# Kernel optimization log

Measured on AMD Instinct MI355X. Metric: run time of the kernel, lower is better.

## Reference

```python
import jax, jax.numpy as jnp
import numpy as np

N, D, H, E = 50000, 128, 128, 800000

def _layernorm(h, g, b, eps=1e-5):
    m = jnp.mean(h, axis=-1, keepdims=True)
    v = jnp.mean((h - m) ** 2, axis=-1, keepdims=True)
    return (h - m) * jax.lax.rsqrt(v + eps) * g + b

def setup_inputs() -> dict:
    key = jax.random.key(0)
    ks = jax.random.split(key, 24)
    s = 0.02
    inp = {
        "x": jax.random.normal(ks[0], (N, D), dtype=jnp.float32),
        "edge_index": jax.random.randint(ks[1], (2, E), 0, N, dtype=jnp.int64),
        "degree": jax.random.uniform(ks[2], (N, 1), dtype=jnp.float32) * 32.0,
        "W_lin": jax.random.normal(ks[3], (D, H), jnp.float32) * s,
        "b_lin": jnp.zeros((H,), jnp.float32),
        "Wa1": jax.random.normal(ks[4], (H, H), jnp.float32) * s,
        "ba1": jnp.zeros((H,), jnp.float32),
        "Wa2": jax.random.normal(ks[5], (H, H), jnp.float32) * s,
        "ba2": jnp.zeros((H,), jnp.float32),
        "Wb1": jax.random.normal(ks[6], (H, H), jnp.float32) * s,
        "bb1": jnp.zeros((H,), jnp.float32),
        "Wb2": jax.random.normal(ks[7], (H, H), jnp.float32) * s,
        "bb2": jnp.zeros((H,), jnp.float32),
        "Wg1": jax.random.normal(ks[8], (H, H), jnp.float32) * s,
        "bg1": jnp.zeros((H,), jnp.float32),
        "Wg2": jax.random.normal(ks[9], (H, H), jnp.float32) * s,
        "bg2": jnp.zeros((H,), jnp.float32),
        "Wf1": jax.random.normal(ks[10], (H, H), jnp.float32) * s,
        "bf1": jnp.zeros((H,), jnp.float32),
        "Wf2": jax.random.normal(ks[11], (H, H), jnp.float32) * s,
        "bf2": jnp.zeros((H,), jnp.float32),
        "ln_g": jnp.ones((H,), jnp.float32),
        "ln_b": jnp.zeros((H,), jnp.float32),
    }
    return inp

def reference(x, edge_index, degree, W_lin, b_lin, Wa1, ba1, Wa2, ba2,
              Wb1, bb1, Wb2, bb2, Wg1, bg1, Wg2, bg2, Wf1, bf1, Wf2, bf2,
              ln_g, ln_b):
    # Dropout layers are identity (eval mode)
    h = x @ W_lin + b_lin                                  # [N,H]
    x_res = _layernorm(h, ln_g, ln_b)
    alpha = jax.nn.softplus(jax.nn.relu(h @ Wa1 + ba1) @ Wa2 + ba2)
    beta = jax.nn.softplus(jax.nn.relu(h @ Wb1 + bb1) @ Wb2 + bb2)
    gamma = jax.nn.gelu(h @ Wg1 + bg1, approximate=False) @ Wg2 + bg2
    src, dst = edge_index[0], edge_index[1]
    agg = jax.ops.segment_sum(h[src], dst, num_segments=h.shape[0])  # [N,H]
    y = (beta * agg + gamma) / (alpha + beta * degree)
    z = jax.nn.gelu(y @ Wf1 + bf1, approximate=False) @ Wf2 + bf2
    return z + x_res
```

## Files before the change

kernel.cpp:

```cpp
#include <hip/hip_runtime.h>
#include <hip/hip_bf16.h>
#include <math.h>

#define NODES 50000
#define NEDGE 800000
#define NT_TILES 782
#define NBUCK 98
#define BSHIFT 9
#define BCAP 10240
#define NP1 195
#define EPB1 4104

typedef __bf16 bf16_t;
typedef __bf16 bf16x8 __attribute__((ext_vector_type(8)));
typedef float floatx4 __attribute__((ext_vector_type(4)));

__device__ __forceinline__ float bfbits2f(unsigned int hi16) {
    union { unsigned int u; float f; } c; c.u = hi16; return c.f;
}
__device__ __forceinline__ unsigned short f2bfbits(float f) {
    bf16_t b = (bf16_t)f; unsigned short u;
    __builtin_memcpy(&u, &b, 2); return u;
}

__device__ __forceinline__ float act_rt(float v, int act) {
    if (act == 1) return fmaxf(v, 0.f);
    if (act == 2) {
        float w = 0.79788456f * (v + 0.044715f * v * v * v);
        float e = __expf(2.f * w);
        float th = 1.f - 2.f / (e + 1.f);
        return 0.5f * v * (1.f + th);
    }
    if (act == 3) return fmaxf(v, 0.f) + __logf(1.f + __expf(-fabsf(v)));
    return v;
}

__global__ __launch_bounds__(256) void prep_w_zero(
    const float* __restrict__ w0, const float* __restrict__ w1,
    const float* __restrict__ w2, const float* __restrict__ w3,
    const float* __restrict__ w4, const float* __restrict__ w5,
    const float* __restrict__ w6, const float* __restrict__ w7,
    const float* __restrict__ w8, bf16_t* __restrict__ wt,
    int* __restrict__ gcur)
{
    if (blockIdx.x >= 9) {
        if (threadIdx.x < NBUCK) gcur[threadIdx.x] = 0;
        return;
    }
    const float* Ws[9] = {w0, w1, w2, w3, w4, w5, w6, w7, w8};
    const float* W = Ws[blockIdx.x];
    bf16_t* o = wt + blockIdx.x * 16384;
    for (int idx = threadIdx.x; idx < 16384; idx += 256) {
        int k = idx >> 7, n = idx & 127;
        o[n * 128 + k] = (bf16_t)W[idx];
    }
}

__device__ __forceinline__ void load_w_regs(const bf16_t* __restrict__ W,
                                            uint4 (&wr)[8], int t)
{
    for (int i = 0; i < 8; ++i) {
        int c = t + i * 256;
        int row = c >> 4, g = c & 15;
        wr[i] = *(const uint4*)(W + row * 128 + g * 8);
    }
}
__device__ __forceinline__ void store_w_regs(const uint4 (&wr)[8],
                                             bf16_t* Bs, int t)
{
    for (int i = 0; i < 8; ++i) {
        int c = t + i * 256;
        int row = c >> 4, g = c & 15;
        *(uint4*)&Bs[row * 128 + ((g ^ (row & 15)) * 8)] = wr[i];
    }
}
__device__ __forceinline__ void afrag_gbf16(const bf16_t* __restrict__ A,
        bf16x8 (&af)[4], int r0, int lane, int wave, int M)
{
    int gr = r0 + wave * 16 + (lane & 15);
    gr = min(gr, M - 1);
    const bf16_t* p = A + (size_t)gr * 128 + (lane >> 4) * 8;
    for (int kc = 0; kc < 4; ++kc)
        af[kc] = *(const bf16x8*)(p + kc * 32);
}
__device__ __forceinline__ void kloop64(const bf16x8 (&af)[4], const bf16_t* Bs,
                                        floatx4 (&acc)[8], int l15, int quad)
{
    for (int ni = 0; ni < 8; ++ni)
        for (int r = 0; r < 4; ++r) acc[ni][r] = 0.f;
    for (int kc = 0; kc < 4; ++kc) {
        int kg = kc * 4 + quad;
        bf16x8 b[8];
        for (int ni = 0; ni < 8; ++ni) {
            int row = ni * 16 + l15;
            b[ni] = *(const bf16x8*)&Bs[row * 128 + ((kg ^ l15) * 8)];
        }
        for (int ni = 0; ni < 8; ++ni)
            acc[ni] = __builtin_amdgcn_mfma_f32_16x16x32_bf16(
                af[kc], b[ni], acc[ni], 0, 0, 0);
    }
}
__device__ __forceinline__ void write_Csw(bf16_t* Csw, floatx4 (&acc)[8],
        const float (&bias_r)[8], int lane, int wave, int act)
{
    const int l15 = lane & 15, quad = lane >> 4;
    for (int ni = 0; ni < 8; ++ni) {
        int col = ni * 16 + l15;
        for (int r = 0; r < 4; ++r) {
            int row = wave * 16 + quad * 4 + r;
            float v = act_rt(acc[ni][r] + bias_r[ni], act);
            Csw[row * 128 + (((col >> 3) ^ (row & 15)) << 3) + (col & 7)] = (bf16_t)v;
        }
    }
}
__device__ __forceinline__ void afrag_Csw(const bf16_t* Csw, bf16x8 (&af)[4],
                                          int lane, int wave)
{
    int l15 = lane & 15, quad = lane >> 4;
    int row = wave * 16 + l15;
    for (int kc = 0; kc < 4; ++kc) {
        int kg = kc * 4 + quad;
        af[kc] = *(const bf16x8*)&Csw[row * 128 + ((kg ^ l15) * 8)];
    }
}
__device__ __forceinline__ void copy_Csw_out(const bf16_t* Csw,
        bf16_t* __restrict__ out, int t, int r0, int M)
{
    for (int i = 0; i < 4; ++i) {
        int c = t + i * 256;
        int row = c >> 4, g = c & 15;
        int gr = r0 + row;
        if (gr < M)
            *(uint4*)(out + (size_t)gr * 128 + g * 8) =
                *(const uint4*)&Csw[row * 128 + ((g ^ (row & 15)) * 8)];
    }
}

__global__ __launch_bounds__(256, 3) void hln_p1(
    const float* __restrict__ x, const bf16_t* __restrict__ wt,
    const float* __restrict__ b_lin,
    const float* __restrict__ ln_g, const float* __restrict__ ln_b,
    bf16_t* __restrict__ h, bf16_t* __restrict__ xres,
    const int* __restrict__ ei, int* __restrict__ gcur,
    unsigned* __restrict__ ebuf, int M)
{
    __shared__ __align__(16) char smem[49152];
    const int t = threadIdx.x;
    const int bid = blockIdx.x;

    if (bid % 5 == 4) {
        int* lcnt  = (int*)smem;
        int* lbase = lcnt + NBUCK;
        if (t < NBUCK) lcnt[t] = 0;
        __syncthreads();
        int p1id = bid / 5;
        int base = p1id * EPB1;
        int e_end = min(base + EPB1, NEDGE);
        for (int e = base + t; e < e_end; e += 256)
            atomicAdd(&lcnt[ei[NEDGE + e] >> BSHIFT], 1);
        __syncthreads();
        if (t < NBUCK) {
            lbase[t] = atomicAdd(&gcur[t], lcnt[t]);
            lcnt[t] = 0;
        }
        __syncthreads();
        for (int e = base + t; e < e_end; e += 256) {
            int d = ei[NEDGE + e];
            int s = ei[e];
            int b = d >> BSHIFT;
            int off = atomicAdd(&lcnt[b], 1);
            int pos = lbase[b] + off;
            if (pos < BCAP)
                ebuf[(size_t)b * BCAP + pos] =
                    (unsigned)s | ((unsigned)(d & 511) << 16);
        }
        return;
    }

    bf16_t* Bs  = (bf16_t*)smem;
    bf16_t* Csw = (bf16_t*)(smem + 32768);
    const int tile = bid - bid / 5;
    const int r0 = tile * 64;
    const int lane = t & 63, wave = t >> 6, l15 = lane & 15, quad = lane >> 4;
    uint4 wr[8];
    bf16x8 af[4];
    floatx4 acc[8];
    float bias_r[8];
    for (int ni = 0; ni < 8; ++ni) bias_r[ni] = b_lin[ni * 16 + l15];

    {
        int gr = min(r0 + wave * 16 + l15, M - 1);
        const float* p = x + (size_t)gr * 128 + quad * 8;
        for (int kc = 0; kc < 4; ++kc) {
            float4 u0 = *(const float4*)(p + kc * 32);
            float4 u1 = *(const float4*)(p + kc * 32 + 4);
            bf16x8 f;
            f[0] = (bf16_t)u0.x; f[1] = (bf16_t)u0.y;
            f[2] = (bf16_t)u0.z; f[3] = (bf16_t)u0.w;
            f[4] = (bf16_t)u1.x; f[5] = (bf16_t)u1.y;
            f[6] = (bf16_t)u1.z; f[7] = (bf16_t)u1.w;
            af[kc] = f;
        }
    }
    load_w_regs(wt, wr, t);
    store_w_regs(wr, Bs, t);
    __syncthreads();
    kloop64(af, Bs, acc, l15, quad);
    write_Csw(Csw, acc, bias_r, lane, wave, 0);
    __syncthreads();

    int row = t >> 2, p4 = t & 3;
    int gr = r0 + row;
    uint4 raw[4];
    float vals[32];
    float s = 0.f, sq = 0.f;
    for (int i = 0; i < 4; ++i) {
        int lg = p4 * 4 + i;
        raw[i] = *(const uint4*)&Csw[row * 128 + ((lg ^ (row & 15)) * 8)];
        const unsigned* u = (const unsigned*)&raw[i];
        for (int k = 0; k < 4; ++k) {
            float f0 = bfbits2f(u[k] << 16);
            float f1 = bfbits2f(u[k] & 0xffff0000u);
            vals[i * 8 + k * 2] = f0; vals[i * 8 + k * 2 + 1] = f1;
            s += f0 + f1; sq += f0 * f0 + f1 * f1;
        }
    }
    s += __shfl_xor(s, 1, 64);  sq += __shfl_xor(sq, 1, 64);
    s += __shfl_xor(s, 2, 64);  sq += __shfl_xor(sq, 2, 64);
    float m   = s * (1.f / 128.f);
    float var = fmaxf(sq * (1.f / 128.f) - m * m, 0.f);
    float rs  = rsqrtf(var + 1e-5f);
    if (gr < M) {
        for (int i = 0; i < 4; ++i) {
            int lg = p4 * 4 + i;
            *(uint4*)(h + (size_t)gr * 128 + lg * 8) = raw[i];
            unsigned short ob[8];
            for (int k = 0; k < 8; ++k) {
                int col = lg * 8 + k;
                ob[k] = f2bfbits((vals[i * 8 + k] - m) * rs * ln_g[col] + ln_b[col]);
            }
            uint4 o;
            o.x = ob[0] | ((unsigned)ob[1] << 16);
            o.y = ob[2] | ((unsigned)ob[3] << 16);
            o.z = ob[4] | ((unsigned)ob[5] << 16);
            o.w = ob[6] | ((unsigned)ob[7] << 16);
            *(uint4*)(xres + (size_t)gr * 128 + lg * 8) = o;
        }
    }
}

__global__ __launch_bounds__(256, 3) void branch_p2(
    const bf16_t* __restrict__ h, const bf16_t* __restrict__ wt,
    const float* __restrict__ ba1, const float* __restrict__ ba2,
    const float* __restrict__ bb1, const float* __restrict__ bb2,
    const float* __restrict__ bg1, const float* __restrict__ bg2,
    bf16_t* __restrict__ al, bf16_t* __restrict__ be, bf16_t* __restrict__ ga,
    const int* __restrict__ gcur, const unsigned* __restrict__ ebuf,
    int* __restrict__ off_start, int* __restrict__ cntN,
    int* __restrict__ srcs, int M)
{
    __shared__ __align__(16) char smem[49152];
    const int t = threadIdx.x;
    const int bid = blockIdx.x;

    if (bid % 25 == 24) {
        int* ncnt = (int*)smem;
        int* sa   = ncnt + 512;
        int* sb   = sa + 512;
        int* ncur = sb + 512;
        int* red  = ncur + 512;
        const int b = bid / 25;
        int total = min(gcur[b], BCAP);

        int v = 0;
        for (int j = t; j < b; j += 256) v += min(gcur[j], BCAP);
        for (int o = 1; o < 64; o <<= 1) v += __shfl_xor(v, o, 64);
        if ((t & 63) == 0) red[t >> 6] = v;
        ncnt[t] = 0; ncnt[t + 256] = 0;
        __syncthreads();
        int bucketBase = red[0] + red[1] + red[2] + red[3];

        const unsigned* eb = ebuf + (size_t)b * BCAP;
        for (int i = t; i < total; i += 256)
            atomicAdd(&ncnt[eb[i] >> 16], 1);
        __syncthreads();
        sa[t] = ncnt[t]; sa[t + 256] = ncnt[t + 256];
        __syncthreads();
        int* pin = sa; int* pout = sb;
        for (int o = 1; o < 512; o <<= 1) {
            for (int j = t; j < 512; j += 256)
                pout[j] = pin[j] + (j >= o ? pin[j - o] : 0);
            __syncthreads();
            int* tmp = pin; pin = pout; pout = tmp;
        }
        for (int j = t; j < 512; j += 256) {
            int excl = pin[j] - ncnt[j];
            int node = (b << BSHIFT) + j;
            if (node < NODES) {
                off_start[node] = bucketBase + excl;
                cntN[node] = ncnt[j];
            }
            ncur[j] = excl;
        }
        __syncthreads();
        for (int i = t; i < total; i += 256) {
            unsigned p = eb[i];
            int dl = p >> 16;
            int pos = atomicAdd(&ncur[dl], 1);
            srcs[bucketBase + pos] = (int)(p & 0xFFFFu);
        }
        return;
    }

    const int tile = bid - bid / 25;
    if (tile >= 3 * NT_TILES) return;
    bf16_t* Bs  = (bf16_t*)smem;
    bf16_t* Csw = (bf16_t*)(smem + 32768);
    const int branch = tile / NT_TILES;
    const int r0 = (tile % NT_TILES) * 64;
    const int lane = t & 63, wave = t >> 6, l15 = lane & 15, quad = lane >> 4;
    uint4 wr[8];
    bf16x8 af[4];
    floatx4 acc[8];

    const bf16_t* w1 = wt + (1 + 2 * branch) * 16384;
    const bf16_t* w2 = wt + (2 + 2 * branch) * 16384;
    const float* b1p = (branch == 0) ? ba1 : (branch == 1) ? bb1 : bg1;
    const float* b2p = (branch == 0) ? ba2 : (branch == 1) ? bb2 : bg2;
    bf16_t* out = (branch == 0) ? al : (branch == 1) ? be : ga;
    const int act1 = (branch == 2) ? 2 : 1;
    const int act2 = (branch == 2) ? 0 : 3;

    float b1_r[8], b2_r[8];
    for (int ni = 0; ni < 8; ++ni) {
        b1_r[ni] = b1p[ni * 16 + l15];
        b2_r[ni] = b2p[ni * 16 + l15];
    }

    afrag_gbf16(h, af, r0, lane, wave, M);
    load_w_regs(w1, wr, t);
    store_w_regs(wr, Bs, t);
    load_w_regs(w2, wr, t);
    __syncthreads();

    kloop64(af, Bs, acc, l15, quad);
    write_Csw(Csw, acc, b1_r, lane, wave, act1);
    __syncthreads();
    store_w_regs(wr, Bs, t);
    __syncthreads();

    afrag_Csw(Csw, af, lane, wave);
    kloop64(af, Bs, acc, l15, quad);
    __syncthreads();
    write_Csw(Csw, acc, b2_r, lane, wave, act2);
    __syncthreads();
    copy_Csw_out(Csw, out, t, r0, M);
}

__global__ __launch_bounds__(256, 3) void fused_out(
    const bf16_t* __restrict__ y, const bf16_t* __restrict__ wt,
    const float* __restrict__ bf1, const float* __restrict__ bf2,
    const bf16_t* __restrict__ xres, float* __restrict__ out, int M)
{
    __shared__ __align__(16) char smem[49152];
    bf16_t* Bs  = (bf16_t*)smem;
    bf16_t* Csw = (bf16_t*)(smem + 32768);
    float*  Cf  = (float*)smem;
    const int t = threadIdx.x;
    const int r0 = blockIdx.x * 64;
    const int lane = t & 63, wave = t >> 6, l15 = lane & 15, quad = lane >> 4;
    uint4 wr[8];
    bf16x8 af[4];
    floatx4 acc[8];

    float b1_r[8], b2_r[8];
    for (int ni = 0; ni < 8; ++ni) {
        b1_r[ni] = bf1[ni * 16 + l15];
        b2_r[ni] = bf2[ni * 16 + l15];
    }

    afrag_gbf16(y, af, r0, lane, wave, M);
    load_w_regs(wt + 7 * 16384, wr, t);
    store_w_regs(wr, Bs, t);
    load_w_regs(wt + 8 * 16384, wr, t);
    __syncthreads();

    kloop64(af, Bs, acc, l15, quad);
    write_Csw(Csw, acc, b1_r, lane, wave, 2);
    __syncthreads();
    store_w_regs(wr, Bs, t);
    __syncthreads();

    afrag_Csw(Csw, af, lane, wave);
    kloop64(af, Bs, acc, l15, quad);
    __syncthreads();

    for (int ni = 0; ni < 8; ++ni) {
        int col = ni * 16 + l15;
        for (int r = 0; r < 4; ++r) {
            int row = wave * 16 + quad * 4 + r;
            Cf[row * 132 + col] = acc[ni][r] + b2_r[ni];
        }
    }
    __syncthreads();
    for (int i = 0; i < 8; ++i) {
        int c = t + i * 256;
        int row = c >> 5, q = c & 31;
        int gr = r0 + row;
        if (gr < M) {
            float4 v = *(const float4*)&Cf[row * 132 + q * 4];
            uint2 xr = *(const uint2*)(xres + (size_t)gr * 128 + q * 4);
            v.x += bfbits2f(xr.x << 16);
            v.y += bfbits2f(xr.x & 0xffff0000u);
            v.z += bfbits2f(xr.y << 16);
            v.w += bfbits2f(xr.y & 0xffff0000u);
            *(float4*)(out + (size_t)gr * 128 + q * 4) = v;
        }
    }
}

__global__ __launch_bounds__(256) void gather_y_kernel(
    const int* __restrict__ off_start, const int* __restrict__ cnt,
    const int* __restrict__ srcs, const bf16_t* __restrict__ h,
    const bf16_t* __restrict__ al, const bf16_t* __restrict__ be,
    const bf16_t* __restrict__ ga, const float* __restrict__ deg,
    bf16_t* __restrict__ y, int M)
{
    int wave = threadIdx.x >> 6, lane = threadIdx.x & 63;
    int node = blockIdx.x * 4 + wave;
    if (node >= M) return;
    int s0 = __builtin_amdgcn_readfirstlane(off_start[node]);
    int n  = __builtin_amdgcn_readfirstlane(cnt[node]);
    int grp = lane >> 4, c16 = lane & 15;
    float a[8] = {0.f, 0.f, 0.f, 0.f, 0.f, 0.f, 0.f, 0.f};

    for (int j = 0; j < n; j += 8) {
        int e0 = j + grp, e1 = j + 4 + grp;
        int i0 = srcs[s0 + min(e0, n - 1)];
        int i1 = srcs[s0 + min(e1, n - 1)];
        uint4 v0 = *(const uint4*)(h + (size_t)i0 * 128 + c16 * 8);
        uint4 v1 = *(const uint4*)(h + (size_t)i1 * 128 + c16 * 8);
        if (e0 < n) {
            const unsigned* u = (const unsigned*)&v0;
            for (int k = 0; k < 4; ++k) {
                a[2 * k]     += bfbits2f(u[k] << 16);
                a[2 * k + 1] += bfbits2f(u[k] & 0xffff0000u);
            }
        }
        if (e1 < n) {
            const unsigned* u = (const unsigned*)&v1;
            for (int k = 0; k < 4; ++k) {
                a[2 * k]     += bfbits2f(u[k] << 16);
                a[2 * k + 1] += bfbits2f(u[k] & 0xffff0000u);
            }
        }
    }
    for (int k = 0; k < 8; ++k) {
        a[k] += __shfl_xor(a[k], 16, 64);
        a[k] += __shfl_xor(a[k], 32, 64);
    }
    if (lane < 16) {
        size_t i0 = (size_t)node * 128 + (size_t)c16 * 8;
        uint4 ra = *(const uint4*)(al + i0);
        uint4 rb = *(const uint4*)(be + i0);
        uint4 rg = *(const uint4*)(ga + i0);
        float d = deg[node];
        const unsigned* ua = (const unsigned*)&ra;
        const unsigned* ub = (const unsigned*)&rb;
        const unsigned* ug = (const unsigned*)&rg;
        unsigned short o[8];
        for (int k = 0; k < 4; ++k) {
            float a0 = bfbits2f(ua[k] << 16), a1 = bfbits2f(ua[k] & 0xffff0000u);
            float b0 = bfbits2f(ub[k] << 16), b1 = bfbits2f(ub[k] & 0xffff0000u);
            float g0 = bfbits2f(ug[k] << 16), g1 = bfbits2f(ug[k] & 0xffff0000u);
            o[2 * k]     = f2bfbits((b0 * a[2 * k]     + g0) / (a0 + b0 * d));
            o[2 * k + 1] = f2bfbits((b1 * a[2 * k + 1] + g1) / (a1 + b1 * d));
        }
        uint4 ov;
        ov.x = o[0] | ((unsigned)o[1] << 16);
        ov.y = o[2] | ((unsigned)o[3] << 16);
        ov.z = o[4] | ((unsigned)o[5] << 16);
        ov.w = o[6] | ((unsigned)o[7] << 16);
        *(uint4*)(y + i0) = ov;
    }
}

extern "C" void kernel_launch(void* const* d_in, const int* in_sizes, int n_in,
                              void* d_out, int out_size, void* d_ws, size_t ws_size,
                              hipStream_t stream)
{
    const float* x    = (const float*)d_in[0];
    const int*   ei   = (const int*)d_in[1];
    const float* deg  = (const float*)d_in[2];
    const float* W_lin = (const float*)d_in[3];  const float* b_lin = (const float*)d_in[4];
    const float* Wa1 = (const float*)d_in[5];    const float* ba1 = (const float*)d_in[6];
    const float* Wa2 = (const float*)d_in[7];    const float* ba2 = (const float*)d_in[8];
    const float* Wb1 = (const float*)d_in[9];    const float* bb1 = (const float*)d_in[10];
    const float* Wb2 = (const float*)d_in[11];   const float* bb2 = (const float*)d_in[12];
    const float* Wg1 = (const float*)d_in[13];   const float* bg1 = (const float*)d_in[14];
    const float* Wg2 = (const float*)d_in[15];   const float* bg2 = (const float*)d_in[16];
    const float* Wf1 = (const float*)d_in[17];   const float* bf1 = (const float*)d_in[18];
    const float* Wf2 = (const float*)d_in[19];   const float* bf2 = (const float*)d_in[20];
    const float* ln_g = (const float*)d_in[21];  const float* ln_b = (const float*)d_in[22];

    const int M = NODES;
    const size_t NB2 = (size_t)M * 128 * 2;

    char* ws = (char*)d_ws;
    size_t off = 0;
    bf16_t* wt  = (bf16_t*)(ws + off); off += (size_t)9 * 16384 * 2;
    bf16_t* h   = (bf16_t*)(ws + off); off += NB2;
    bf16_t* al  = (bf16_t*)(ws + off); off += NB2;
    bf16_t* be  = (bf16_t*)(ws + off); off += NB2;
    bf16_t* ga  = (bf16_t*)(ws + off); off += NB2;
    bf16_t* yv  = (bf16_t*)(ws + off); off += NB2;
    bf16_t* xres = (bf16_t*)(ws + off); off += NB2;
    int* gcur      = (int*)(ws + off); off += 128 * 4;
    int* off_start = (int*)(ws + off); off += (size_t)NODES * 4 + 64;
    int* cntN      = (int*)(ws + off); off += (size_t)NODES * 4 + 64;
    int* srcs      = (int*)(ws + off); off += (size_t)NEDGE * 4;
    unsigned* ebuf = (unsigned*)(ws + off); off += (size_t)NBUCK * BCAP * 4;
    float* outp = (float*)d_out;

    dim3 blk(256);

    prep_w_zero<<<10, blk, 0, stream>>>(
        W_lin, Wa1, Wa2, Wb1, Wb2, Wg1, Wg2, Wf1, Wf2, wt, gcur);

    hln_p1<<<977, blk, 0, stream>>>(
        x, wt, b_lin, ln_g, ln_b, h, xres, ei, gcur, ebuf, M);

    branch_p2<<<2450, blk, 0, stream>>>(
        h, wt, ba1, ba2, bb1, bb2, bg1, bg2, al, be, ga,
        gcur, ebuf, off_start, cntN, srcs, M);

    gather_y_kernel<<<(M + 3) / 4, blk, 0, stream>>>(off_start, cntN, srcs, h,
                                                     al, be, ga, deg, yv, M);
    fused_out<<<NT_TILES, blk, 0, stream>>>(yv, wt, bf1, bf2, xres, outp, M);
}
```

Measured before the change: 282.2 us.

## Co-schedule alpha/beta branch MLPs with edge gather; fuse y computation into output GEMM

Restructures the kernel schedule. The CSR build now runs together with only the gamma branch MLP. The alpha and beta branch tiles are interleaved with the neighbor-gather blocks in one launch, so the MMA-heavy tiles overlap the memory-bound gather. The y = (beta*agg+gamma)/(alpha+beta*deg) combine moves into the output GEMM's A-fragment load. The gather now writes an fp32 agg buffer instead of a bf16 y, which doubles that intermediate's traffic but removes the separate y pass.

```diff
diff --git a/kernel.cpp b/kernel.cpp
--- a/kernel.cpp
+++ b/kernel.cpp
@@ -8,7 +8,6 @@
 #define NBUCK 98
 #define BSHIFT 9
 #define BCAP 10240
-#define NP1 195
 #define EPB1 4104
 
 typedef __bf16 bf16_t;
@@ -134,6 +133,56 @@
             *(uint4*)(out + (size_t)gr * 128 + g * 8) =
                 *(const uint4*)&Csw[row * 128 + ((g ^ (row & 15)) * 8)];
     }
+}
+
+__device__ __forceinline__ void branch_tile_body(
+    char* smem, int t, int br, int r0,
+    const bf16_t* __restrict__ h, const bf16_t* __restrict__ wt,
+    const float* __restrict__ ba1, const float* __restrict__ ba2,
+    const float* __restrict__ bb1, const float* __restrict__ bb2,
+    const float* __restrict__ bg1, const float* __restrict__ bg2,
+    bf16_t* __restrict__ al, bf16_t* __restrict__ be, bf16_t* __restrict__ ga,
+    int M)
+{
+    bf16_t* Bs  = (bf16_t*)smem;
+    bf16_t* Csw = (bf16_t*)(smem + 32768);
+    const int lane = t & 63, wave = t >> 6, l15 = lane & 15, quad = lane >> 4;
+    uint4 wr[8];
+    bf16x8 af[4];
+    floatx4 acc[8];
+
+    const bf16_t* w1 = wt + (1 + 2 * br) * 16384;
+    const bf16_t* w2 = wt + (2 + 2 * br) * 16384;
+    const float* b1p = (br == 0) ? ba1 : (br == 1) ? bb1 : bg1;
+    const float* b2p = (br == 0) ? ba2 : (br == 1) ? bb2 : bg2;
+    bf16_t* out = (br == 0) ? al : (br == 1) ? be : ga;
+    const int act1 = (br == 2) ? 2 : 1;
+    const int act2 = (br == 2) ? 0 : 3;
+
+    float b1_r[8], b2_r[8];
+    for (int ni = 0; ni < 8; ++ni) {
+        b1_r[ni] = b1p[ni * 16 + l15];
+        b2_r[ni] = b2p[ni * 16 + l15];
+    }
+
+    afrag_gbf16(h, af, r0, lane, wave, M);
+    load_w_regs(w1, wr, t);
+    store_w_regs(wr, Bs, t);
+    load_w_regs(w2, wr, t);
+    __syncthreads();
+
+    kloop64(af, Bs, acc, l15, quad);
+    write_Csw(Csw, acc, b1_r, lane, wave, act1);
+    __syncthreads();
+    store_w_regs(wr, Bs, t);
+    __syncthreads();
+
+    afrag_Csw(Csw, af, lane, wave);
+    kloop64(af, Bs, acc, l15, quad);
+    __syncthreads();
+    write_Csw(Csw, acc, b2_r, lane, wave, act2);
+    __syncthreads();
+    copy_Csw_out(Csw, out, t, r0, M);
 }
 
 __global__ __launch_bounds__(256, 3) void hln_p1(
@@ -249,7 +298,7 @@
     }
 }
 
-__global__ __launch_bounds__(256, 3) void branch_p2(
+__global__ __launch_bounds__(256, 3) void p2_gamma(
     const bf16_t* __restrict__ h, const bf16_t* __restrict__ wt,
     const float* __restrict__ ba1, const float* __restrict__ ba2,
     const float* __restrict__ bb1, const float* __restrict__ bb2,
@@ -263,13 +312,13 @@
     const int t = threadIdx.x;
     const int bid = blockIdx.x;
 
-    if (bid % 25 == 24) {
+    if (bid < NBUCK) {
         int* ncnt = (int*)smem;
         int* sa   = ncnt + 512;
         int* sb   = sa + 512;
         int* ncur = sb + 512;
         int* red  = ncur + 512;
-        const int b = bid / 25;
+        const int b = bid;
         int total = min(gcur[b], BCAP);
 
         int v = 0;
@@ -312,53 +361,75 @@
         return;
     }
 
-    const int tile = bid - bid / 25;
-    if (tile >= 3 * NT_TILES) return;
-    bf16_t* Bs  = (bf16_t*)smem;
-    bf16_t* Csw = (bf16_t*)(smem + 32768);
-    const int branch = tile / NT_TILES;
-    const int r0 = (tile % NT_TILES) * 64;
-    const int lane = t & 63, wave = t >> 6, l15 = lane & 15, quad = lane >> 4;
-    uint4 wr[8];
-    bf16x8 af[4];
-    floatx4 acc[8];
-
-    const bf16_t* w1 = wt + (1 + 2 * branch) * 16384;
-    const bf16_t* w2 = wt + (2 + 2 * branch) * 16384;
-    const float* b1p = (branch == 0) ? ba1 : (branch == 1) ? bb1 : bg1;
-    const float* b2p = (branch == 0) ? ba2 : (branch == 1) ? bb2 : bg2;
-    bf16_t* out = (branch == 0) ? al : (branch == 1) ? be : ga;
-    const int act1 = (branch == 2) ? 2 : 1;
-    const int act2 = (branch == 2) ? 0 : 3;
-
-    float b1_r[8], b2_r[8];
-    for (int ni = 0; ni < 8; ++ni) {
-        b1_r[ni] = b1p[ni * 16 + l15];
-        b2_r[ni] = b2p[ni * 16 + l15];
-    }
-
-    afrag_gbf16(h, af, r0, lane, wave, M);
-    load_w_regs(w1, wr, t);
-    store_w_regs(wr, Bs, t);
-    load_w_regs(w2, wr, t);
-    __syncthreads();
-
-    kloop64(af, Bs, acc, l15, quad);
-    write_Csw(Csw, acc, b1_r, lane, wave, act1);
-    __syncthreads();
-    store_w_regs(wr, Bs, t);
-    __syncthreads();
-
-    afrag_Csw(Csw, af, lane, wave);
-    kloop64(af, Bs, acc, l15, quad);
-    __syncthreads();
-    write_Csw(Csw, acc, b2_r, lane, wave, act2);
-    __syncthreads();
-    copy_Csw_out(Csw, out, t, r0, M);
-}
-
-__global__ __launch_bounds__(256, 3) void fused_out(
-    const bf16_t* __restrict__ y, const bf16_t* __restrict__ wt,
+    branch_tile_body(smem, t, 2, (bid - NBUCK) * 64,
+                     h, wt, ba1, ba2, bb1, bb2, bg1, bg2, al, be, ga, M);
+}
+
+__global__ __launch_bounds__(256, 3) void branchAB_gather(
+    const bf16_t* __restrict__ h, const bf16_t* __restrict__ wt,
+    const float* __restrict__ ba1, const float* __restrict__ ba2,
+    const float* __restrict__ bb1, const float* __restrict__ bb2,
+    const float* __restrict__ bg1, const float* __restrict__ bg2,
+    bf16_t* __restrict__ al, bf16_t* __restrict__ be, bf16_t* __restrict__ ga,
+    const int* __restrict__ off_start, const int* __restrict__ cntN,
+    const int* __restrict__ srcs, float* __restrict__ agg, int M)
+{
+    __shared__ __align__(16) char smem[49152];
+    const int t = threadIdx.x;
+    const int bid = blockIdx.x;
+
+    if (bid % 9 == 0) {
+        int tile = bid / 9;
+        branch_tile_body(smem, t, tile / NT_TILES, (tile % NT_TILES) * 64,
+                         h, wt, ba1, ba2, bb1, bb2, bg1, bg2, al, be, ga, M);
+        return;
+    }
+
+    int gb = (bid / 9) * 8 + (bid % 9) - 1;
+    int wave = t >> 6, lane = t & 63;
+    int node = gb * 4 + wave;
+    if (node >= M) return;
+    int s0 = __builtin_amdgcn_readfirstlane(off_start[node]);
+    int n  = __builtin_amdgcn_readfirstlane(cntN[node]);
+    int grp = lane >> 4, c16 = lane & 15;
+    float a[8] = {0.f, 0.f, 0.f, 0.f, 0.f, 0.f, 0.f, 0.f};
+
+    for (int j = 0; j < n; j += 8) {
+        int e0 = j + grp, e1 = j + 4 + grp;
+        int i0 = srcs[s0 + min(e0, n - 1)];
+        int i1 = srcs[s0 + min(e1, n - 1)];
+        uint4 v0 = *(const uint4*)(h + (size_t)i0 * 128 + c16 * 8);
+        uint4 v1 = *(const uint4*)(h + (size_t)i1 * 128 + c16 * 8);
+        if (e0 < n) {
+            const unsigned* u = (const unsigned*)&v0;
+            for (int k = 0; k < 4; ++k) {
+                a[2 * k]     += bfbits2f(u[k] << 16);
+                a[2 * k + 1] += bfbits2f(u[k] & 0xffff0000u);
+            }
+        }
+        if (e1 < n) {
+            const unsigned* u = (const unsigned*)&v1;
+            for (int k = 0; k < 4; ++k) {
+                a[2 * k]     += bfbits2f(u[k] << 16);
+                a[2 * k + 1] += bfbits2f(u[k] & 0xffff0000u);
+            }
+        }
+    }
+    for (int k = 0; k < 8; ++k) {
+        a[k] += __shfl_xor(a[k], 16, 64);
+        a[k] += __shfl_xor(a[k], 32, 64);
+    }
+    if (lane < 16) {
+        float* p = agg + (size_t)node * 128 + (size_t)c16 * 8;
+        *(float4*)(p)     = make_float4(a[0], a[1], a[2], a[3]);
+        *(float4*)(p + 4) = make_float4(a[4], a[5], a[6], a[7]);
+    }
+}
+
+__global__ __launch_bounds__(256, 3) void y_out(
+    const float* __restrict__ agg, const bf16_t* __restrict__ al,
+    const bf16_t* __restrict__ be, const bf16_t* __restrict__ ga,
+    const float* __restrict__ deg, const bf16_t* __restrict__ wt,
     const float* __restrict__ bf1, const float* __restrict__ bf2,
     const bf16_t* __restrict__ xres, float* __restrict__ out, int M)
 {
@@ -379,7 +450,32 @@
         b2_r[ni] = bf2[ni * 16 + l15];
     }
 
-    afrag_gbf16(y, af, r0, lane, wave, M);
+    {
+        int gr = min(r0 + wave * 16 + l15, M - 1);
+        float d = deg[gr];
+        for (int kc = 0; kc < 4; ++kc) {
+            int cb = kc * 32 + quad * 8;
+            uint4 ua = *(const uint4*)(al + (size_t)gr * 128 + cb);
+            uint4 ub = *(const uint4*)(be + (size_t)gr * 128 + cb);
+            uint4 ug = *(const uint4*)(ga + (size_t)gr * 128 + cb);
+            float4 q0 = *(const float4*)(agg + (size_t)gr * 128 + cb);
+            float4 q1 = *(const float4*)(agg + (size_t)gr * 128 + cb + 4);
+            float av[8] = {q0.x, q0.y, q0.z, q0.w, q1.x, q1.y, q1.z, q1.w};
+            const unsigned* pa = (const unsigned*)&ua;
+            const unsigned* pb = (const unsigned*)&ub;
+            const unsigned* pg = (const unsigned*)&ug;
+            bf16x8 f;
+            for (int k = 0; k < 4; ++k) {
+                float a0 = bfbits2f(pa[k] << 16), a1 = bfbits2f(pa[k] & 0xffff0000u);
+                float b0 = bfbits2f(pb[k] << 16), b1 = bfbits2f(pb[k] & 0xffff0000u);
+                float g0 = bfbits2f(pg[k] << 16), g1 = bfbits2f(pg[k] & 0xffff0000u);
+                f[2 * k]     = (bf16_t)((b0 * av[2 * k]     + g0) / (a0 + b0 * d));
+                f[2 * k + 1] = (bf16_t)((b1 * av[2 * k + 1] + g1) / (a1 + b1 * d));
+            }
+            af[kc] = f;
+        }
+    }
+
     load_w_regs(wt + 7 * 16384, wr, t);
     store_w_regs(wr, Bs, t);
     load_w_regs(wt + 8 * 16384, wr, t);
@@ -416,72 +512,6 @@
             v.w += bfbits2f(xr.y & 0xffff0000u);
             *(float4*)(out + (size_t)gr * 128 + q * 4) = v;
         }
-    }
-}
-
-__global__ __launch_bounds__(256) void gather_y_kernel(
-    const int* __restrict__ off_start, const int* __restrict__ cnt,
-    const int* __restrict__ srcs, const bf16_t* __restrict__ h,
-    const bf16_t* __restrict__ al, const bf16_t* __restrict__ be,
-    const bf16_t* __restrict__ ga, const float* __restrict__ deg,
-    bf16_t* __restrict__ y, int M)
-{
-    int wave = threadIdx.x >> 6, lane = threadIdx.x & 63;
-    int node = blockIdx.x * 4 + wave;
-    if (node >= M) return;
-    int s0 = __builtin_amdgcn_readfirstlane(off_start[node]);
-    int n  = __builtin_amdgcn_readfirstlane(cnt[node]);
-    int grp = lane >> 4, c16 = lane & 15;
-    float a[8] = {0.f, 0.f, 0.f, 0.f, 0.f, 0.f, 0.f, 0.f};
-
-    for (int j = 0; j < n; j += 8) {
-        int e0 = j + grp, e1 = j + 4 + grp;
-        int i0 = srcs[s0 + min(e0, n - 1)];
-        int i1 = srcs[s0 + min(e1, n - 1)];
-        uint4 v0 = *(const uint4*)(h + (size_t)i0 * 128 + c16 * 8);
-        uint4 v1 = *(const uint4*)(h + (size_t)i1 * 128 + c16 * 8);
-        if (e0 < n) {
-            const unsigned* u = (const unsigned*)&v0;
-            for (int k = 0; k < 4; ++k) {
-                a[2 * k]     += bfbits2f(u[k] << 16);
-                a[2 * k + 1] += bfbits2f(u[k] & 0xffff0000u);
-            }
-        }
-        if (e1 < n) {
-            const unsigned* u = (const unsigned*)&v1;
-            for (int k = 0; k < 4; ++k) {
-                a[2 * k]     += bfbits2f(u[k] << 16);
-                a[2 * k + 1] += bfbits2f(u[k] & 0xffff0000u);
-            }
-        }
-    }
-    for (int k = 0; k < 8; ++k) {
-        a[k] += __shfl_xor(a[k], 16, 64);
-        a[k] += __shfl_xor(a[k], 32, 64);
-    }
-    if (lane < 16) {
-        size_t i0 = (size_t)node * 128 + (size_t)c16 * 8;
-        uint4 ra = *(const uint4*)(al + i0);
-        uint4 rb = *(const uint4*)(be + i0);
-        uint4 rg = *(const uint4*)(ga + i0);
-        float d = deg[node];
-        const unsigned* ua = (const unsigned*)&ra;
-        const unsigned* ub = (const unsigned*)&rb;
-        const unsigned* ug = (const unsigned*)&rg;
-        unsigned short o[8];
-        for (int k = 0; k < 4; ++k) {
-            float a0 = bfbits2f(ua[k] << 16), a1 = bfbits2f(ua[k] & 0xffff0000u);
-            float b0 = bfbits2f(ub[k] << 16), b1 = bfbits2f(ub[k] & 0xffff0000u);
-            float g0 = bfbits2f(ug[k] << 16), g1 = bfbits2f(ug[k] & 0xffff0000u);
-            o[2 * k]     = f2bfbits((b0 * a[2 * k]     + g0) / (a0 + b0 * d));
-            o[2 * k + 1] = f2bfbits((b1 * a[2 * k + 1] + g1) / (a1 + b1 * d));
-        }
-        uint4 ov;
-        ov.x = o[0] | ((unsigned)o[1] << 16);
-        ov.y = o[2] | ((unsigned)o[3] << 16);
-        ov.z = o[4] | ((unsigned)o[5] << 16);
-        ov.w = o[6] | ((unsigned)o[7] << 16);
-        *(uint4*)(y + i0) = ov;
     }
 }
 
@@ -505,6 +535,7 @@
 
     const int M = NODES;
     const size_t NB2 = (size_t)M * 128 * 2;
+    const size_t NB4 = (size_t)M * 128 * 4;
 
     char* ws = (char*)d_ws;
     size_t off = 0;
@@ -513,8 +544,8 @@
     bf16_t* al  = (bf16_t*)(ws + off); off += NB2;
     bf16_t* be  = (bf16_t*)(ws + off); off += NB2;
     bf16_t* ga  = (bf16_t*)(ws + off); off += NB2;
-    bf16_t* yv  = (bf16_t*)(ws + off); off += NB2;
     bf16_t* xres = (bf16_t*)(ws + off); off += NB2;
+    float*  agg  = (float*)(ws + off); off += NB4;
     int* gcur      = (int*)(ws + off); off += 128 * 4;
     int* off_start = (int*)(ws + off); off += (size_t)NODES * 4 + 64;
     int* cntN      = (int*)(ws + off); off += (size_t)NODES * 4 + 64;
@@ -530,11 +561,14 @@
     hln_p1<<<977, blk, 0, stream>>>(
         x, wt, b_lin, ln_g, ln_b, h, xres, ei, gcur, ebuf, M);
 
-    branch_p2<<<2450, blk, 0, stream>>>(
+    p2_gamma<<<NBUCK + NT_TILES, blk, 0, stream>>>(
         h, wt, ba1, ba2, bb1, bb2, bg1, bg2, al, be, ga,
         gcur, ebuf, off_start, cntN, srcs, M);
 
-    gather_y_kernel<<<(M + 3) / 4, blk, 0, stream>>>(off_start, cntN, srcs, h,
-                                                     al, be, ga, deg, yv, M);
-    fused_out<<<NT_TILES, blk, 0, stream>>>(yv, wt, bf1, bf2, xres, outp, M);
-}
+    branchAB_gather<<<9 * 1564, blk, 0, stream>>>(
+        h, wt, ba1, ba2, bb1, bb2, bg1, bg2, al, be, ga,
+        off_start, cntN, srcs, agg, M);
+
+    y_out<<<NT_TILES, blk, 0, stream>>>(
+        agg, al, be, ga, deg, wt, bf1, bf2, xres, outp, M);
+}
```

Measured after the change: 316.9 us. 12.3% more time.
